# Performance work log

Hardware: AMD Instinct MI355X
Metric: run time of the kernel (lower is better)

## Reference

```python
import jax, jax.numpy as jnp
import numpy as np

B = 256          # batch size
S_DIM = 512      # signalDimension
L_DIM = 2048     # latentDimension
SF = L_DIM // S_DIM   # scaleFactor = 4
NSIG = 50        # numSignals
LN_EPS = 1e-10


def _conv1d(x, w, b, dil=1):
    """Conv1d with reflect 'same' padding. x:(B,Cin,L) w:(Cout,Cin,K) b:(Cout,)."""
    k = w.shape[-1]
    pad = dil * (k - 1) // 2
    xp = jnp.pad(x, ((0, 0), (0, 0), (pad, pad)), mode='reflect')
    y = jax.lax.conv_general_dilated(
        xp, w, window_strides=(1,), padding='VALID', rhs_dilation=(dil,),
        dimension_numbers=('NCH', 'OIH', 'NCH'))
    return y + b[None, :, None]


def setup_inputs() -> dict:
    key = jax.random.key(0)
    ks = jax.random.split(key, 8)

    def w(k, shape, fan_in):
        return jax.random.normal(k, shape, jnp.float32) / np.float32(np.sqrt(fan_in))

    return {
        'latentData': jax.random.normal(ks[0], (B, L_DIM), jnp.float32),
        # sharedCNN: Conv1d(SF->2SF,k5,d1) SELU Conv1d(2SF->SF,k5,d2)
        'shared_w1': w(ks[1], (2 * SF, SF, 5), SF * 5),
        'shared_b1': jnp.zeros((2 * SF,), jnp.float32),
        'shared_w2': w(ks[2], (SF, 2 * SF, 5), 2 * SF * 5),
        'shared_b2': jnp.zeros((SF,), jnp.float32),
        # initialLayerNorm over signalDimension
        'ln_g': jnp.ones((S_DIM,), jnp.float32),
        'ln_b': jnp.zeros((S_DIM,), jnp.float32),
        # per-signal channelReduction_CNN stacks (stacked over NSIG):
        # Conv1d(SF->8,k7,d1) Conv1d(8->4,k5,d1) SELU Conv1d(4->2,k5,d1) Conv1d(2->1,k5,d2) SELU
        'sig_w1': w(ks[3], (NSIG, 8, SF, 7), SF * 7),
        'sig_b1': jnp.zeros((NSIG, 8), jnp.float32),
        'sig_w2': w(ks[4], (NSIG, 4, 8, 5), 8 * 5),
        'sig_b2': jnp.zeros((NSIG, 4), jnp.float32),
        'sig_w3': w(ks[5], (NSIG, 2, 4, 5), 4 * 5),
        'sig_b3': jnp.zeros((NSIG, 2), jnp.float32),
        'sig_w4': w(ks[6], (NSIG, 1, 2, 5), 2 * 5),
        'sig_b4': jnp.zeros((NSIG, 1), jnp.float32),
    }


def reference(latentData, shared_w1, shared_b1, shared_w2, shared_b2,
              ln_g, ln_b, sig_w1, sig_b1, sig_w2, sig_b2,
              sig_w3, sig_b3, sig_w4, sig_b4):
    b = latentData.shape[0]
    # (B, latentDim) -> (B, signalDim, SF) -> (B, SF, signalDim)
    x = latentData.reshape(b, S_DIM, SF).transpose(0, 2, 1)

    def shared(h):
        h = jax.nn.selu(_conv1d(h, shared_w1, shared_b1, dil=1))
        return _conv1d(h, shared_w2, shared_b2, dil=2)

    d = shared(shared(x)) + x  # two passes of sharedCNN + residual
    # LayerNorm over last axis (signalDimension), eps=1e-10
    mu = jnp.mean(d, axis=-1, keepdims=True)
    var = jnp.mean((d - mu) ** 2, axis=-1, keepdims=True)
    d = (d - mu) / jnp.sqrt(var + LN_EPS) * ln_g + ln_b

    def one_signal(w1, b1, w2, b2, w3, b3, w4, b4):
        h = _conv1d(d, w1, b1, dil=1)            # (B,8,L)
        h = jax.nn.selu(_conv1d(h, w2, b2, 1))   # (B,4,L)
        h = _conv1d(h, w3, b3, dil=1)            # (B,2,L)
        h = jax.nn.selu(_conv1d(h, w4, b4, 2))   # (B,1,L)
        return h[:, 0, :]                        # (B,L)

    # vectorize the 50-signal Python loop via vmap over stacked weights
    y = jax.vmap(one_signal)(sig_w1, sig_b1, sig_w2, sig_b2,
                             sig_w3, sig_b3, sig_w4, sig_b4)  # (NSIG,B,L)
    return y.transpose(1, 0, 2)  # (B, NSIG, signalDim)
```

## Files before the change

### kernel.cpp

```cpp
#include <hip/hip_runtime.h>
#include <math.h>

#define BB 256
#define L 512
#define NSIG 50
#define PAD 4
#define STR (L + 2 * PAD)

__device__ __forceinline__ int refl(int i) {
    if (i < 0) i = -i;
    if (i >= L) i = 2 * L - 2 - i;
    return i;
}

__device__ __forceinline__ float selu(float x) {
    const float scale = 1.0507009873554804934193349852946f;
    const float alpha = 1.6732632423543772848170429916717f;
    return x > 0.f ? scale * x : scale * alpha * (__expf(x) - 1.f);
}

__global__ __launch_bounds__(256) void shared_ln_kernel(
    const float* __restrict__ latent,
    const float* __restrict__ w1, const float* __restrict__ b1,
    const float* __restrict__ w2, const float* __restrict__ b2,
    const float* __restrict__ g,  const float* __restrict__ beta,
    float* __restrict__ D)
{
    __shared__ float xb[4][L];
    __shared__ float hb[8][L];
    __shared__ float yb[4][L];
    __shared__ float sw1[160], sb1[8], sw2[160], sb2[4];

    const int b = blockIdx.x;
    const int t = threadIdx.x;

    for (int i = t; i < 160; i += 256) { sw1[i] = w1[i]; sw2[i] = w2[i]; }
    if (t < 8) sb1[t] = b1[t];
    if (t < 4) sb2[t] = b2[t];

    const float* lp = latent + (size_t)b * 2048;
    for (int i = t; i < 2048; i += 256)
        xb[i & 3][i >> 2] = lp[i];
    __syncthreads();

    for (int pass = 0; pass < 2; ++pass) {
        const float (*src)[L] = (pass == 0) ? (const float (*)[L])xb
                                            : (const float (*)[L])yb;
        for (int idx = t; idx < 8 * L; idx += 256) {
            int co = idx >> 9, l = idx & (L - 1);
            float acc = sb1[co];
            #pragma unroll
            for (int ci = 0; ci < 4; ++ci) {
                const float* w = &sw1[(co * 4 + ci) * 5];
                #pragma unroll
                for (int k = 0; k < 5; ++k)
                    acc += w[k] * src[ci][refl(l + k - 2)];
            }
            hb[co][l] = selu(acc);
        }
        __syncthreads();
        for (int idx = t; idx < 4 * L; idx += 256) {
            int co = idx >> 9, l = idx & (L - 1);
            float acc = sb2[co];
            #pragma unroll
            for (int ci = 0; ci < 8; ++ci) {
                const float* w = &sw2[(co * 8 + ci) * 5];
                #pragma unroll
                for (int k = 0; k < 5; ++k)
                    acc += w[k] * hb[ci][refl(l + 2 * k - 4)];
            }
            if (pass == 1) acc += xb[co][l];
            yb[co][l] = acc;
        }
        __syncthreads();
    }

    const int wave = t >> 6;
    const int lane = t & 63;
    float v[8];
    float s = 0.f;
    #pragma unroll
    for (int j = 0; j < 8; ++j) { v[j] = yb[wave][lane * 8 + j]; s += v[j]; }
    #pragma unroll
    for (int off = 32; off > 0; off >>= 1) s += __shfl_down(s, off);
    s = __shfl(s, 0);
    const float mu = s * (1.f / 512.f);
    float s2 = 0.f;
    #pragma unroll
    for (int j = 0; j < 8; ++j) { float d = v[j] - mu; s2 += d * d; }
    #pragma unroll
    for (int off = 32; off > 0; off >>= 1) s2 += __shfl_down(s2, off);
    s2 = __shfl(s2, 0);
    const float rinv = rsqrtf(s2 * (1.f / 512.f) + 1e-10f);

    float* Dp = D + ((size_t)b * 4 + wave) * L;
    #pragma unroll
    for (int j = 0; j < 8; ++j) {
        int l = lane * 8 + j;
        Dp[l] = (v[j] - mu) * rinv * g[l] + beta[l];
    }
}

__global__ __launch_bounds__(128) void signal_kernel(
    const float* __restrict__ D,
    const float* __restrict__ w1, const float* __restrict__ b1,
    const float* __restrict__ w2, const float* __restrict__ b2,
    const float* __restrict__ w3, const float* __restrict__ b3,
    const float* __restrict__ w4, const float* __restrict__ b4,
    float* __restrict__ out)
{
    const int s = blockIdx.x;
    const int b = blockIdx.y;
    const int t = threadIdx.x;
    const int p0 = t * 4;

    __shared__ float bufA[4][STR];
    __shared__ float bufB[8][STR];

    const float* W1 = w1 + s * 224; const float* B1 = b1 + s * 8;
    const float* W2 = w2 + s * 160; const float* B2 = b2 + s * 4;
    const float* W3 = w3 + s * 40;  const float* B3 = b3 + s * 2;
    const float* W4 = w4 + s * 10;

    {
        const float4* Dv = (const float4*)(D + (size_t)b * 2048);
        #pragma unroll
        for (int j = 0; j < 4; ++j) {
            int i = t + j * 128;
            float4 v = Dv[i];
            int c = i >> 7, col = (i & 127) << 2;
            *(float4*)&bufA[c][PAD + col] = v;
        }
    }
    __syncthreads();
    if (t < 32) {
        int r = t >> 3, j = t & 7;
        if (j < 4) bufA[r][PAD - 1 - j] = bufA[r][PAD + 1 + j];
        else { int i = j - 4; bufA[r][PAD + L + i] = bufA[r][PAD + L - 2 - i]; }
    }
    __syncthreads();

    {
        float acc[8][4];
        #pragma unroll
        for (int co = 0; co < 8; ++co) {
            float bb = B1[co];
            #pragma unroll
            for (int pp = 0; pp < 4; ++pp) acc[co][pp] = bb;
        }
        #pragma unroll
        for (int ci = 0; ci < 4; ++ci) {
            float x[12];
            const float* row = &bufA[ci][p0];
            *(float4*)&x[0] = *(const float4*)&row[0];
            *(float4*)&x[4] = *(const float4*)&row[4];
            *(float4*)&x[8] = *(const float4*)&row[8];
            #pragma unroll
            for (int co = 0; co < 8; ++co)
                #pragma unroll
                for (int k = 0; k < 7; ++k) {
                    float w = W1[(co * 4 + ci) * 7 + k];
                    #pragma unroll
                    for (int pp = 0; pp < 4; ++pp)
                        acc[co][pp] += w * x[pp + k + 1];
                }
        }
        #pragma unroll
        for (int co = 0; co < 8; ++co) {
            float4 v = { acc[co][0], acc[co][1], acc[co][2], acc[co][3] };
            *(float4*)&bufB[co][PAD + p0] = v;
        }
    }
    __syncthreads();
    if (t < 64) {
        int r = t >> 3, j = t & 7;
        if (j < 4) bufB[r][PAD - 1 - j] = bufB[r][PAD + 1 + j];
        else { int i = j - 4; bufB[r][PAD + L + i] = bufB[r][PAD + L - 2 - i]; }
    }
    __syncthreads();

    {
        float acc[4][4];
        #pragma unroll
        for (int co = 0; co < 4; ++co) {
            float bb = B2[co];
            #pragma unroll
            for (int pp = 0; pp < 4; ++pp) acc[co][pp] = bb;
        }
        #pragma unroll
        for (int ci = 0; ci < 8; ++ci) {
            float x[8];
            const float* row = &bufB[ci][p0 + 2];
            *(float2*)&x[0] = *(const float2*)&row[0];
            *(float4*)&x[2] = *(const float4*)&row[2];
            *(float2*)&x[6] = *(const float2*)&row[6];
            #pragma unroll
            for (int co = 0; co < 4; ++co)
                #pragma unroll
                for (int k = 0; k < 5; ++k) {
                    float w = W2[(co * 8 + ci) * 5 + k];
                    #pragma unroll
                    for (int pp = 0; pp < 4; ++pp)
                        acc[co][pp] += w * x[pp + k];
                }
        }
        #pragma unroll
        for (int co = 0; co < 4; ++co) {
            float4 v = { selu(acc[co][0]), selu(acc[co][1]),
                         selu(acc[co][2]), selu(acc[co][3]) };
            *(float4*)&bufA[co][PAD + p0] = v;
        }
    }
    __syncthreads();
    if (t < 32) {
        int r = t >> 3, j = t & 7;
        if (j < 4) bufA[r][PAD - 1 - j] = bufA[r][PAD + 1 + j];
        else { int i = j - 4; bufA[r][PAD + L + i] = bufA[r][PAD + L - 2 - i]; }
    }
    __syncthreads();

    {
        float acc[2][4];
        #pragma unroll
        for (int co = 0; co < 2; ++co) {
            float bb = B3[co];
            #pragma unroll
            for (int pp = 0; pp < 4; ++pp) acc[co][pp] = bb;
        }
        #pragma unroll
        for (int ci = 0; ci < 4; ++ci) {
            float x[8];
            const float* row = &bufA[ci][p0 + 2];
            *(float2*)&x[0] = *(const float2*)&row[0];
            *(float4*)&x[2] = *(const float4*)&row[2];
            *(float2*)&x[6] = *(const float2*)&row[6];
            #pragma unroll
            for (int co = 0; co < 2; ++co)
                #pragma unroll
                for (int k = 0; k < 5; ++k) {
                    float w = W3[(co * 4 + ci) * 5 + k];
                    #pragma unroll
                    for (int pp = 0; pp < 4; ++pp)
                        acc[co][pp] += w * x[pp + k];
                }
        }
        #pragma unroll
        for (int co = 0; co < 2; ++co) {
            float4 v = { acc[co][0], acc[co][1], acc[co][2], acc[co][3] };
            *(float4*)&bufB[co][PAD + p0] = v;
        }
    }
    __syncthreads();
    if (t < 16) {
        int r = t >> 3, j = t & 7;
        if (j < 4) bufB[r][PAD - 1 - j] = bufB[r][PAD + 1 + j];
        else { int i = j - 4; bufB[r][PAD + L + i] = bufB[r][PAD + L - 2 - i]; }
    }
    __syncthreads();

    {
        float acc[4];
        float bb = b4[s];
        #pragma unroll
        for (int pp = 0; pp < 4; ++pp) acc[pp] = bb;
        #pragma unroll
        for (int ci = 0; ci < 2; ++ci) {
            float x[12];
            const float* row = &bufB[ci][p0];
            *(float4*)&x[0] = *(const float4*)&row[0];
            *(float4*)&x[4] = *(const float4*)&row[4];
            *(float4*)&x[8] = *(const float4*)&row[8];
            #pragma unroll
            for (int k = 0; k < 5; ++k) {
                float w = W4[ci * 5 + k];
                #pragma unroll
                for (int pp = 0; pp < 4; ++pp)
                    acc[pp] += w * x[pp + 2 * k];
            }
        }
        float4 r = { selu(acc[0]), selu(acc[1]), selu(acc[2]), selu(acc[3]) };
        *(float4*)&out[((size_t)b * NSIG + s) * L + p0] = r;
    }
}

extern "C" void kernel_launch(void* const* d_in, const int* in_sizes, int n_in,
                              void* d_out, int out_size, void* d_ws, size_t ws_size,
                              hipStream_t stream) {
    const float* latent = (const float*)d_in[0];
    const float* sw1 = (const float*)d_in[1];
    const float* sb1 = (const float*)d_in[2];
    const float* sw2 = (const float*)d_in[3];
    const float* sb2 = (const float*)d_in[4];
    const float* ln_g = (const float*)d_in[5];
    const float* ln_b = (const float*)d_in[6];
    const float* g_w1 = (const float*)d_in[7];
    const float* g_b1 = (const float*)d_in[8];
    const float* g_w2 = (const float*)d_in[9];
    const float* g_b2 = (const float*)d_in[10];
    const float* g_w3 = (const float*)d_in[11];
    const float* g_b3 = (const float*)d_in[12];
    const float* g_w4 = (const float*)d_in[13];
    const float* g_b4 = (const float*)d_in[14];
    float* out = (float*)d_out;
    float* D = (float*)d_ws;

    shared_ln_kernel<<<BB, 256, 0, stream>>>(latent, sw1, sb1, sw2, sb2,
                                             ln_g, ln_b, D);
    signal_kernel<<<dim3(NSIG, BB), 128, 0, stream>>>(D, g_w1, g_b1, g_w2, g_b2,
                                                      g_w3, g_b3, g_w4, g_b4, out);
}
```

Measured before the change: 121.3 us.

## Restructure signal kernel: 256 threads, split conv1 channels, fused halo writes

The signal kernel moves from 128 to 256 threads per block, with each thread producing 2 outputs instead of 4. Conv1's 8 output channels are computed in two halves of 4 that feed conv2 as partial sums, so shared memory shrinks from 12 to 8 rows. Reflect halos are now written inline by the edge threads, which removes the separate halo passes and their extra barriers. The aim is lower register and LDS pressure for higher occupancy and less synchronization, at the cost of more threads and smaller per-thread reuse of loaded values.

```diff
diff --git a/kernel.cpp b/kernel.cpp
--- a/kernel.cpp
+++ b/kernel.cpp
@@ -17,6 +17,17 @@
     const float scale = 1.0507009873554804934193349852946f;
     const float alpha = 1.6732632423543772848170429916717f;
     return x > 0.f ? scale * x : scale * alpha * (__expf(x) - 1.f);
+}
+
+__device__ __forceinline__ void halo_w(float* row, int t, float v0, float v1, int W) {
+    if (t == 0)               row[PAD - 1] = v1;
+    if (t == 1) {             row[PAD - 2] = v0;
+        if (W >= 3)           row[PAD - 3] = v1; }
+    if (t == 2 && W >= 4)     row[PAD - 4] = v0;
+    if (t == 255)             row[PAD + L] = v0;
+    if (t == 254) {           row[PAD + L + 1] = v1;
+        if (W >= 3)           row[PAD + L + 2] = v0; }
+    if (t == 253 && W >= 4)   row[PAD + L + 3] = v1;
 }
 
 __global__ __launch_bounds__(256) void shared_ln_kernel(
@@ -101,7 +112,7 @@
     }
 }
 
-__global__ __launch_bounds__(128) void signal_kernel(
+__global__ __launch_bounds__(256, 8) void signal_kernel(
     const float* __restrict__ D,
     const float* __restrict__ w1, const float* __restrict__ b1,
     const float* __restrict__ w2, const float* __restrict__ b2,
@@ -112,10 +123,10 @@
     const int s = blockIdx.x;
     const int b = blockIdx.y;
     const int t = threadIdx.x;
-    const int p0 = t * 4;
-
-    __shared__ float bufA[4][STR];
-    __shared__ float bufB[8][STR];
+    const int p0 = t * 2;
+
+    __shared__ float Xb[4][STR];
+    __shared__ float Yb[4][STR];
 
     const float* W1 = w1 + s * 224; const float* B1 = b1 + s * 8;
     const float* W2 = w2 + s * 160; const float* B2 = b2 + s * 4;
@@ -125,161 +136,143 @@
     {
         const float4* Dv = (const float4*)(D + (size_t)b * 2048);
         #pragma unroll
-        for (int j = 0; j < 4; ++j) {
-            int i = t + j * 128;
+        for (int j = 0; j < 2; ++j) {
+            int i = t + j * 256;
             float4 v = Dv[i];
             int c = i >> 7, col = (i & 127) << 2;
-            *(float4*)&bufA[c][PAD + col] = v;
+            *(float4*)&Xb[c][PAD + col] = v;
+            if ((i & 127) == 0) {
+                Xb[c][PAD - 1] = v.y; Xb[c][PAD - 2] = v.z; Xb[c][PAD - 3] = v.w;
+            }
+            if ((i & 127) == 127) {
+                Xb[c][PAD + L] = v.z; Xb[c][PAD + L + 1] = v.y; Xb[c][PAD + L + 2] = v.x;
+            }
         }
     }
     __syncthreads();
-    if (t < 32) {
-        int r = t >> 3, j = t & 7;
-        if (j < 4) bufA[r][PAD - 1 - j] = bufA[r][PAD + 1 + j];
-        else { int i = j - 4; bufA[r][PAD + L + i] = bufA[r][PAD + L - 2 - i]; }
+
+    float acc2[4][2];
+    #pragma unroll
+    for (int co = 0; co < 4; ++co) {
+        float bb = B2[co];
+        acc2[co][0] = bb; acc2[co][1] = bb;
+    }
+
+    #pragma unroll
+    for (int half = 0; half < 2; ++half) {
+        float a1[4][2];
+        #pragma unroll
+        for (int co = 0; co < 4; ++co) {
+            float bb = B1[half * 4 + co];
+            a1[co][0] = bb; a1[co][1] = bb;
+        }
+        #pragma unroll
+        for (int ci = 0; ci < 4; ++ci) {
+            float x[10];
+            const float* row = &Xb[ci][p0];
+            *(float2*)&x[0] = *(const float2*)&row[0];
+            *(float2*)&x[2] = *(const float2*)&row[2];
+            *(float2*)&x[4] = *(const float2*)&row[4];
+            *(float2*)&x[6] = *(const float2*)&row[6];
+            *(float2*)&x[8] = *(const float2*)&row[8];
+            #pragma unroll
+            for (int co = 0; co < 4; ++co)
+                #pragma unroll
+                for (int k = 0; k < 7; ++k) {
+                    float w = W1[((half * 4 + co) * 4 + ci) * 7 + k];
+                    a1[co][0] += w * x[k + 1];
+                    a1[co][1] += w * x[k + 2];
+                }
+        }
+        if (half == 1) __syncthreads();
+        #pragma unroll
+        for (int co = 0; co < 4; ++co) {
+            float2 v = { a1[co][0], a1[co][1] };
+            *(float2*)&Yb[co][PAD + p0] = v;
+            halo_w(Yb[co], t, v.x, v.y, 2);
+        }
+        __syncthreads();
+
+        #pragma unroll
+        for (int ci = 0; ci < 4; ++ci) {
+            float x[8];
+            const float* row = &Yb[ci][p0 + 2];
+            *(float2*)&x[0] = *(const float2*)&row[0];
+            *(float2*)&x[2] = *(const float2*)&row[2];
+            *(float2*)&x[4] = *(const float2*)&row[4];
+            *(float2*)&x[6] = *(const float2*)&row[6];
+            #pragma unroll
+            for (int co = 0; co < 4; ++co)
+                #pragma unroll
+                for (int k = 0; k < 5; ++k) {
+                    float w = W2[(co * 8 + half * 4 + ci) * 5 + k];
+                    acc2[co][0] += w * x[k];
+                    acc2[co][1] += w * x[k + 1];
+                }
+        }
+    }
+
+    #pragma unroll
+    for (int co = 0; co < 4; ++co) {
+        float2 v = { selu(acc2[co][0]), selu(acc2[co][1]) };
+        *(float2*)&Xb[co][PAD + p0] = v;
+        halo_w(Xb[co], t, v.x, v.y, 2);
     }
     __syncthreads();
 
     {
-        float acc[8][4];
-        #pragma unroll
-        for (int co = 0; co < 8; ++co) {
-            float bb = B1[co];
-            #pragma unroll
-            for (int pp = 0; pp < 4; ++pp) acc[co][pp] = bb;
-        }
-        #pragma unroll
-        for (int ci = 0; ci < 4; ++ci) {
-            float x[12];
-            const float* row = &bufA[ci][p0];
-            *(float4*)&x[0] = *(const float4*)&row[0];
-            *(float4*)&x[4] = *(const float4*)&row[4];
-            *(float4*)&x[8] = *(const float4*)&row[8];
-            #pragma unroll
-            for (int co = 0; co < 8; ++co)
-                #pragma unroll
-                for (int k = 0; k < 7; ++k) {
-                    float w = W1[(co * 4 + ci) * 7 + k];
-                    #pragma unroll
-                    for (int pp = 0; pp < 4; ++pp)
-                        acc[co][pp] += w * x[pp + k + 1];
-                }
-        }
-        #pragma unroll
-        for (int co = 0; co < 8; ++co) {
-            float4 v = { acc[co][0], acc[co][1], acc[co][2], acc[co][3] };
-            *(float4*)&bufB[co][PAD + p0] = v;
-        }
-    }
-    __syncthreads();
-    if (t < 64) {
-        int r = t >> 3, j = t & 7;
-        if (j < 4) bufB[r][PAD - 1 - j] = bufB[r][PAD + 1 + j];
-        else { int i = j - 4; bufB[r][PAD + L + i] = bufB[r][PAD + L - 2 - i]; }
-    }
-    __syncthreads();
-
-    {
-        float acc[4][4];
-        #pragma unroll
-        for (int co = 0; co < 4; ++co) {
-            float bb = B2[co];
-            #pragma unroll
-            for (int pp = 0; pp < 4; ++pp) acc[co][pp] = bb;
-        }
-        #pragma unroll
-        for (int ci = 0; ci < 8; ++ci) {
-            float x[8];
-            const float* row = &bufB[ci][p0 + 2];
-            *(float2*)&x[0] = *(const float2*)&row[0];
-            *(float4*)&x[2] = *(const float4*)&row[2];
-            *(float2*)&x[6] = *(const float2*)&row[6];
-            #pragma unroll
-            for (int co = 0; co < 4; ++co)
-                #pragma unroll
-                for (int k = 0; k < 5; ++k) {
-                    float w = W2[(co * 8 + ci) * 5 + k];
-                    #pragma unroll
-                    for (int pp = 0; pp < 4; ++pp)
-                        acc[co][pp] += w * x[pp + k];
-                }
-        }
-        #pragma unroll
-        for (int co = 0; co < 4; ++co) {
-            float4 v = { selu(acc[co][0]), selu(acc[co][1]),
-                         selu(acc[co][2]), selu(acc[co][3]) };
-            *(float4*)&bufA[co][PAD + p0] = v;
-        }
-    }
-    __syncthreads();
-    if (t < 32) {
-        int r = t >> 3, j = t & 7;
-        if (j < 4) bufA[r][PAD - 1 - j] = bufA[r][PAD + 1 + j];
-        else { int i = j - 4; bufA[r][PAD + L + i] = bufA[r][PAD + L - 2 - i]; }
-    }
-    __syncthreads();
-
-    {
-        float acc[2][4];
+        float a3[2][2];
         #pragma unroll
         for (int co = 0; co < 2; ++co) {
             float bb = B3[co];
-            #pragma unroll
-            for (int pp = 0; pp < 4; ++pp) acc[co][pp] = bb;
+            a3[co][0] = bb; a3[co][1] = bb;
         }
         #pragma unroll
         for (int ci = 0; ci < 4; ++ci) {
             float x[8];
-            const float* row = &bufA[ci][p0 + 2];
+            const float* row = &Xb[ci][p0 + 2];
             *(float2*)&x[0] = *(const float2*)&row[0];
-            *(float4*)&x[2] = *(const float4*)&row[2];
+            *(float2*)&x[2] = *(const float2*)&row[2];
+            *(float2*)&x[4] = *(const float2*)&row[4];
             *(float2*)&x[6] = *(const float2*)&row[6];
             #pragma unroll
             for (int co = 0; co < 2; ++co)
                 #pragma unroll
                 for (int k = 0; k < 5; ++k) {
                     float w = W3[(co * 4 + ci) * 5 + k];
-                    #pragma unroll
-                    for (int pp = 0; pp < 4; ++pp)
-                        acc[co][pp] += w * x[pp + k];
+                    a3[co][0] += w * x[k];
+                    a3[co][1] += w * x[k + 1];
                 }
         }
         #pragma unroll
         for (int co = 0; co < 2; ++co) {
-            float4 v = { acc[co][0], acc[co][1], acc[co][2], acc[co][3] };
-            *(float4*)&bufB[co][PAD + p0] = v;
+            float2 v = { a3[co][0], a3[co][1] };
+            *(float2*)&Yb[co][PAD + p0] = v;
+            halo_w(Yb[co], t, v.x, v.y, 4);
         }
     }
     __syncthreads();
-    if (t < 16) {
-        int r = t >> 3, j = t & 7;
-        if (j < 4) bufB[r][PAD - 1 - j] = bufB[r][PAD + 1 + j];
-        else { int i = j - 4; bufB[r][PAD + L + i] = bufB[r][PAD + L - 2 - i]; }
-    }
-    __syncthreads();
 
     {
-        float acc[4];
-        float bb = b4[s];
-        #pragma unroll
-        for (int pp = 0; pp < 4; ++pp) acc[pp] = bb;
+        float a0 = b4[s], a1v = a0;
         #pragma unroll
         for (int ci = 0; ci < 2; ++ci) {
-            float x[12];
-            const float* row = &bufB[ci][p0];
-            *(float4*)&x[0] = *(const float4*)&row[0];
-            *(float4*)&x[4] = *(const float4*)&row[4];
-            *(float4*)&x[8] = *(const float4*)&row[8];
+            float x[10];
+            const float* row = &Yb[ci][p0];
+            *(float2*)&x[0] = *(const float2*)&row[0];
+            *(float2*)&x[2] = *(const float2*)&row[2];
+            *(float2*)&x[4] = *(const float2*)&row[4];
+            *(float2*)&x[6] = *(const float2*)&row[6];
+            *(float2*)&x[8] = *(const float2*)&row[8];
             #pragma unroll
             for (int k = 0; k < 5; ++k) {
                 float w = W4[ci * 5 + k];
-                #pragma unroll
-                for (int pp = 0; pp < 4; ++pp)
-                    acc[pp] += w * x[pp + 2 * k];
-            }
-        }
-        float4 r = { selu(acc[0]), selu(acc[1]), selu(acc[2]), selu(acc[3]) };
-        *(float4*)&out[((size_t)b * NSIG + s) * L + p0] = r;
+                a0  += w * x[2 * k];
+                a1v += w * x[2 * k + 1];
+            }
+        }
+        float2 r = { selu(a0), selu(a1v) };
+        *(float2*)&out[((size_t)b * NSIG + s) * L + p0] = r;
     }
 }
 
@@ -306,6 +299,6 @@
 
     shared_ln_kernel<<<BB, 256, 0, stream>>>(latent, sw1, sb1, sw2, sb2,
                                              ln_g, ln_b, D);
-    signal_kernel<<<dim3(NSIG, BB), 128, 0, stream>>>(D, g_w1, g_b1, g_w2, g_b2,
+    signal_kernel<<<dim3(NSIG, BB), 256, 0, stream>>>(D, g_w1, g_b1, g_w2, g_b2,
                                                       g_w3, g_b3, g_w4, g_b4, out);
 }
```

Result: slower. 484.3 us (+299.3%).
